# Kernel tuning notes

Hardware: AMD Instinct MI355X
Metric: run time of the kernel (lower is better)

The kernel has to match this reference:

```python
import jax, jax.numpy as jnp
import numpy as np

L, D, OC, GROUPS, EPS = 256, 1280, 128, 8, 1e-5


def setup_inputs() -> dict:
    key = jax.random.key(0)
    k1, k2 = jax.random.split(key)
    feats = jax.random.normal(k1, (L, D), dtype=jnp.float32)
    # Conv2d(3d, out_ch, kernel_size=1) weight flattened to (out_ch, 3d)
    W = jax.random.normal(k2, (OC, 3 * D), dtype=jnp.float32) * (1.0 / np.sqrt(3 * D))
    b = jnp.zeros((OC,), dtype=jnp.float32)
    gamma = jnp.ones((OC,), dtype=jnp.float32)
    beta = jnp.zeros((OC,), dtype=jnp.float32)
    return {"feats": feats, "W": W, "b": b, "gamma": gamma, "beta": beta}


def reference(feats, W, b, gamma, beta):
    fi = feats[:, None, :]                     # (L, 1, d)
    fj = feats[None, :, :]                     # (1, L, d)
    add = fi + fj                              # (L, L, d)
    diff = jnp.abs(fi - fj)                    # (L, L, d)
    had = fi * fj                              # (L, L, d)
    pair = jnp.concatenate([add, diff, had], axis=-1)  # (L, L, 3d)
    # 1x1 conv == per-pixel linear: (L, L, 3d) x (out_ch, 3d)^T -> (L, L, out_ch)
    x = jnp.einsum('ijc,oc->ijo', pair, W) + b
    # GroupNorm(8, out_ch) on batch=1: normalize over (C/g, L, L) per group
    xg = jnp.transpose(x, (2, 0, 1)).reshape(GROUPS, OC // GROUPS, L, L)
    mean = jnp.mean(xg, axis=(1, 2, 3), keepdims=True)
    var = jnp.var(xg, axis=(1, 2, 3), keepdims=True)
    xn = ((xg - mean) * jax.lax.rsqrt(var + EPS)).reshape(OC, L, L)
    xn = xn * gamma[:, None, None] + beta[:, None, None]
    out = jax.nn.gelu(xn, approximate=False)   # torch nn.GELU default = exact erf
    return out[None]                           # (1, out_ch, L, L)
```

## Files before the change

### kernel.cpp

```cpp
#include <hip/hip_runtime.h>
#include <math.h>

typedef unsigned int uint;
typedef unsigned short ushort;

typedef __attribute__((ext_vector_type(8))) _Float16 f16x8;
typedef __attribute__((ext_vector_type(2))) _Float16 f16x2;
typedef __attribute__((ext_vector_type(16))) float floatx16;

#define NFEAT 327680
#define NW    491520

union U4H8 { uint4 u; f16x8 h; uint w[4]; };

__device__ inline ushort f2h(float f) {
  _Float16 h = (_Float16)f;
  union { _Float16 h; ushort s; } c; c.h = h; return c.s;
}
__device__ inline f16x2 asf16x2(uint u) {
  union { uint u; f16x2 h; } c; c.u = u; return c.h;
}
__device__ inline uint asuint(f16x2 h) {
  union { f16x2 h; uint u; } c; c.h = h; return c.u;
}

__device__ inline void async16(const ushort* g, ushort* l) {
  __builtin_amdgcn_global_load_lds((const __attribute__((address_space(1))) uint*)g,
                                   (__attribute__((address_space(3))) uint*)l, 16, 0, 0);
}

__global__ void prep_kernel(const float* __restrict__ feats,
                            const float* __restrict__ W,
                            ushort* __restrict__ fH,
                            ushort* __restrict__ wH,
                            float* __restrict__ stats,
                            float* __restrict__ Aoi) {
  int idx = blockIdx.x * 256 + threadIdx.x;
  if (blockIdx.x == 0 && threadIdx.x < 16) stats[threadIdx.x] = 0.0f;
  if (idx < 32768) Aoi[idx] = 0.0f;
  if (idx < NFEAT) fH[idx] = f2h(feats[idx]);
  else             wH[idx - NFEAT] = f2h(W[idx - NFEAT]);
}

__global__ __launch_bounds__(256, 2) void gemma_kernel(
    const ushort* __restrict__ fH, const ushort* __restrict__ wH,
    float* __restrict__ Aoi) {
  __shared__ float red[4][1024];
  const int tid = threadIdx.x, lane = tid & 63, w = tid >> 6;
  const int i0 = (blockIdx.x >> 4) << 5;
  const int kq = (blockIdx.x >> 2) & 3;
  const int ot = blockIdx.x & 3;
  const int rr = lane & 31, half = lane >> 5;
  floatx16 a4;
  #pragma unroll
  for (int r = 0; r < 16; ++r) a4[r] = 0.0f;
  const int kbase = kq * 320 + w * 80 + half * 8;
  #pragma unroll
  for (int ks = 0; ks < 5; ++ks) {
    const int k = kbase + ks * 16;
    U4H8 bf; bf.u = *(const uint4*)(fH + (i0 + rr) * 1280 + k);
    U4H8 af; af.u = *(const uint4*)(wH + (ot * 32 + rr) * 3840 + k);
    a4 = __builtin_amdgcn_mfma_f32_32x32x16_f16(af.h, bf.h, a4, 0, 0, 0);
  }
  #pragma unroll
  for (int r = 0; r < 16; ++r) {
    const int orow = (r & 3) + 8 * (r >> 2) + 4 * half;
    red[w][orow * 32 + rr] = a4[r];
  }
  __syncthreads();
  for (int e = tid; e < 1024; e += 256) {
    float s = red[0][e] + red[1][e] + red[2][e] + red[3][e];
    atomicAdd(&Aoi[(ot * 32 + (e >> 5)) * 256 + i0 + (e & 31)], s);
  }
}

__device__ inline void build_pair(const uint4 vj, const uint4 vi, U4H8& d, U4H8& h) {
  const uint ju[4] = {vj.x, vj.y, vj.z, vj.w};
  const uint iu[4] = {vi.x, vi.y, vi.z, vi.w};
  #pragma unroll
  for (int t = 0; t < 4; ++t) {
    f16x2 a = asf16x2(iu[t]);
    f16x2 b = asf16x2(ju[t]);
    f16x2 dd = a - b;
    f16x2 hh = a * b;
    d.w[t] = asuint(dd) & 0x7fff7fffu;
    h.w[t] = asuint(hh);
  }
}

__global__ __launch_bounds__(256, 2) void gemm_kernel(
    const ushort* __restrict__ fH, const ushort* __restrict__ wH,
    const float* __restrict__ bias, const float* __restrict__ Aoi,
    float* __restrict__ xout, float* __restrict__ stats) {
  __shared__ __align__(16) ushort Wl[2 * 128 * 64];

  const int tid = threadIdx.x;
  const int blk = blockIdx.x;
  const int i0 = (blk >> 2) << 1;
  const int j0 = (blk & 3) << 6;
  const int lane = tid & 63;
  const int w = tid >> 6;
  const int wo = (w >> 1) << 6;
  const int wm = (w & 1) << 5;
  const int rr = lane & 31;
  const int half = lane >> 5;
  const int rr7 = lane & 7;

  const ushort* gsrc[4];
  #pragma unroll
  for (int p = 0; p < 4; ++p) {
    const int seg = w * 4 + p;
    const int row = seg * 8 + (lane >> 3);
    const int g = (lane & 7) ^ (lane >> 3);
    gsrc[p] = wH + row * 3840 + 1280 + (g >> 2) * 1280 + (g & 3) * 8;
  }

  const ushort* fi0p = fH + i0 * 1280 + half * 8;
  const ushort* fi1p = fi0p + 1280;
  const ushort* fjp = fH + (j0 + wm + rr) * 1280 + half * 8;

  floatx16 acc[2][2];
  #pragma unroll
  for (int a = 0; a < 2; ++a)
    #pragma unroll
    for (int ot = 0; ot < 2; ++ot)
      #pragma unroll
      for (int r = 0; r < 16; ++r) acc[a][ot][r] = 0.0f;

  #pragma unroll
  for (int p = 0; p < 4; ++p)
    async16(gsrc[p], &Wl[(w * 4 + p) * 512]);
  uint4 vi0[2], vi1[2], vj[2];
  #pragma unroll
  for (int st = 0; st < 2; ++st) {
    vj[st]  = *(const uint4*)(fjp  + st * 16);
    vi0[st] = *(const uint4*)(fi0p + st * 16);
    vi1[st] = *(const uint4*)(fi1p + st * 16);
  }
  __syncthreads();

  for (int cc = 0; cc < 40; ++cc) {
    const ushort* Wc = &Wl[(cc & 1) * 8192];
    uint4 vi0n[2], vi1n[2], vjn[2];
    if (cc < 39) {
      const int cn = (cc + 1) << 5;
      #pragma unroll
      for (int p = 0; p < 4; ++p)
        async16(gsrc[p] + cn, &Wl[((cc & 1) ^ 1) * 8192 + (w * 4 + p) * 512]);
      __builtin_amdgcn_sched_barrier(0);
      #pragma unroll
      for (int st = 0; st < 2; ++st) {
        vjn[st]  = *(const uint4*)(fjp  + cn + st * 16);
        vi0n[st] = *(const uint4*)(fi0p + cn + st * 16);
        vi1n[st] = *(const uint4*)(fi1p + cn + st * 16);
      }
      __builtin_amdgcn_sched_barrier(0);
    }
    #pragma unroll
    for (int st = 0; st < 2; ++st) {
      U4H8 d0, h0, d1, h1;
      build_pair(vj[st], vi0[st], d0, h0);
      build_pair(vj[st], vi1[st], d1, h1);
      const int g0 = (st << 1) + half;
      #pragma unroll
      for (int ot = 0; ot < 2; ++ot) {
        const int rowb = (wo + ot * 32 + rr) << 6;
        f16x8 ad = *(const f16x8*)(Wc + rowb + ((g0 ^ rr7) << 3));
        f16x8 ah = *(const f16x8*)(Wc + rowb + (((g0 + 4) ^ rr7) << 3));
        acc[0][ot] = __builtin_amdgcn_mfma_f32_32x32x16_f16(ad, d0.h, acc[0][ot], 0, 0, 0);
        acc[1][ot] = __builtin_amdgcn_mfma_f32_32x32x16_f16(ad, d1.h, acc[1][ot], 0, 0, 0);
        acc[0][ot] = __builtin_amdgcn_mfma_f32_32x32x16_f16(ah, h0.h, acc[0][ot], 0, 0, 0);
        acc[1][ot] = __builtin_amdgcn_mfma_f32_32x32x16_f16(ah, h1.h, acc[1][ot], 0, 0, 0);
      }
    }
    if (cc < 39) {
      __builtin_amdgcn_sched_barrier(0);
      __builtin_amdgcn_s_waitcnt(0x0F74);
      __builtin_amdgcn_s_barrier();
      __builtin_amdgcn_sched_barrier(0);
      __asm__ volatile("" ::: "memory");
      #pragma unroll
      for (int st = 0; st < 2; ++st) {
        vj[st] = vjn[st]; vi0[st] = vi0n[st]; vi1[st] = vi1n[st];
      }
    }
  }

  float gs[2][2] = {{0.f, 0.f}, {0.f, 0.f}};
  float gq[2][2] = {{0.f, 0.f}, {0.f, 0.f}};
  const int jg = j0 + wm + rr;
  #pragma unroll
  for (int ii = 0; ii < 2; ++ii) {
    const int irow = i0 + ii;
    const int mglob = irow * 256 + jg;
    #pragma unroll
    for (int ot = 0; ot < 2; ++ot) {
      #pragma unroll
      for (int r = 0; r < 16; ++r) {
        const int orow = (r & 3) + 8 * (r >> 2) + 4 * half;
        const int o = wo + ot * 32 + orow;
        float x = acc[ii][ot][r] + Aoi[o * 256 + irow] + Aoi[o * 256 + jg] + bias[o];
        xout[o * 65536 + mglob] = x;
        gs[ot][r >> 3] += x;
        gq[ot][r >> 3] += x * x;
      }
    }
  }
  __syncthreads();
  float* sred = (float*)Wl;
  if (tid < 16) sred[tid] = 0.0f;
  __syncthreads();
  #pragma unroll
  for (int ot = 0; ot < 2; ++ot) {
    #pragma unroll
    for (int rg = 0; rg < 2; ++rg) {
      float s = gs[ot][rg], qv = gq[ot][rg];
      for (int off = 32; off > 0; off >>= 1) {
        s += __shfl_xor(s, off, 64);
        qv += __shfl_xor(qv, off, 64);
      }
      if (lane == 0) {
        const int g = (wo >> 4) + ot * 2 + rg;
        atomicAdd(&sred[g], s);
        atomicAdd(&sred[8 + g], qv);
      }
    }
  }
  __syncthreads();
  if (tid < 16) atomicAdd(&stats[tid], sred[tid]);
}

__global__ void norm_kernel(float* __restrict__ xout,
                            const float* __restrict__ stats,
                            const float* __restrict__ gamma,
                            const float* __restrict__ beta) {
  const int idx = blockIdx.x * 256 + threadIdx.x;
  const int e = idx << 2;
  const int o = e >> 16;
  const int g = o >> 4;
  const float invN = 1.0f / 1048576.0f;
  const float mean = stats[g] * invN;
  const float var = stats[8 + g] * invN - mean * mean;
  const float inv = rsqrtf(var + 1e-5f);
  const float ga = gamma[o], be = beta[o];
  float4 v = *(float4*)(xout + e);
  float* pv = &v.x;
  #pragma unroll
  for (int t = 0; t < 4; ++t) {
    float xn = (pv[t] - mean) * inv * ga + be;
    pv[t] = 0.5f * xn * (1.0f + erff(xn * 0.70710678118654752f));
  }
  *(float4*)(xout + e) = v;
}

extern "C" void kernel_launch(void* const* d_in, const int* in_sizes, int n_in,
                              void* d_out, int out_size, void* d_ws, size_t ws_size,
                              hipStream_t stream) {
  const float* feats = (const float*)d_in[0];
  const float* W     = (const float*)d_in[1];
  const float* bias  = (const float*)d_in[2];
  const float* gamma = (const float*)d_in[3];
  const float* beta  = (const float*)d_in[4];
  float* out = (float*)d_out;

  ushort* fH = (ushort*)d_ws;
  ushort* wH = fH + NFEAT;
  float* stats = (float*)(wH + NW);
  float* Aoi = stats + 16;

  prep_kernel<<<3200, 256, 0, stream>>>(feats, W, fH, wH, stats, Aoi);
  gemma_kernel<<<128, 256, 0, stream>>>(fH, wH, Aoi);
  gemm_kernel<<<512, 256, 0, stream>>>(fH, wH, bias, Aoi, out, stats);
  norm_kernel<<<8192, 256, 0, stream>>>(out, stats, gamma, beta);
}
```

Measured before the change: 146.8 us.

## Halve gemm block tile to 32 columns and raise occupancy to four blocks per CU

Each gemm block now covers 2 rows by 32 columns of j instead of 64, and each of the four waves owns 32 output channels with a single accumulator pair instead of 64 channels split across two warps in the m dimension. The grid doubles to 1024 blocks and launch bounds ask for 4 blocks per CU, cutting accumulator registers so that more waves can be resident and the 256 CUs are better filled. The cost is that each block loads the same full 128x64 weight tile into LDS for half as much output, which doubles total weight traffic and LDS fill per unit of work.

```diff
diff --git a/kernel.cpp b/kernel.cpp
--- a/kernel.cpp
+++ b/kernel.cpp
@@ -88,7 +88,7 @@
   }
 }
 
-__global__ __launch_bounds__(256, 2) void gemm_kernel(
+__global__ __launch_bounds__(256, 4) void gemm_kernel(
     const ushort* __restrict__ fH, const ushort* __restrict__ wH,
     const float* __restrict__ bias, const float* __restrict__ Aoi,
     float* __restrict__ xout, float* __restrict__ stats) {
@@ -96,12 +96,11 @@
 
   const int tid = threadIdx.x;
   const int blk = blockIdx.x;
-  const int i0 = (blk >> 2) << 1;
-  const int j0 = (blk & 3) << 6;
+  const int i0 = (blk >> 3) << 1;
+  const int j0 = (blk & 7) << 5;
   const int lane = tid & 63;
   const int w = tid >> 6;
-  const int wo = (w >> 1) << 6;
-  const int wm = (w & 1) << 5;
+  const int wo = w << 5;
   const int rr = lane & 31;
   const int half = lane >> 5;
   const int rr7 = lane & 7;
@@ -117,15 +116,13 @@
 
   const ushort* fi0p = fH + i0 * 1280 + half * 8;
   const ushort* fi1p = fi0p + 1280;
-  const ushort* fjp = fH + (j0 + wm + rr) * 1280 + half * 8;
-
-  floatx16 acc[2][2];
+  const ushort* fjp = fH + (j0 + rr) * 1280 + half * 8;
+
+  floatx16 acc[2];
   #pragma unroll
   for (int a = 0; a < 2; ++a)
     #pragma unroll
-    for (int ot = 0; ot < 2; ++ot)
-      #pragma unroll
-      for (int r = 0; r < 16; ++r) acc[a][ot][r] = 0.0f;
+    for (int r = 0; r < 16; ++r) acc[a][r] = 0.0f;
 
   #pragma unroll
   for (int p = 0; p < 4; ++p)
@@ -162,16 +159,13 @@
       build_pair(vj[st], vi0[st], d0, h0);
       build_pair(vj[st], vi1[st], d1, h1);
       const int g0 = (st << 1) + half;
-      #pragma unroll
-      for (int ot = 0; ot < 2; ++ot) {
-        const int rowb = (wo + ot * 32 + rr) << 6;
-        f16x8 ad = *(const f16x8*)(Wc + rowb + ((g0 ^ rr7) << 3));
-        f16x8 ah = *(const f16x8*)(Wc + rowb + (((g0 + 4) ^ rr7) << 3));
-        acc[0][ot] = __builtin_amdgcn_mfma_f32_32x32x16_f16(ad, d0.h, acc[0][ot], 0, 0, 0);
-        acc[1][ot] = __builtin_amdgcn_mfma_f32_32x32x16_f16(ad, d1.h, acc[1][ot], 0, 0, 0);
-        acc[0][ot] = __builtin_amdgcn_mfma_f32_32x32x16_f16(ah, h0.h, acc[0][ot], 0, 0, 0);
-        acc[1][ot] = __builtin_amdgcn_mfma_f32_32x32x16_f16(ah, h1.h, acc[1][ot], 0, 0, 0);
-      }
+      const int rowb = (wo + rr) << 6;
+      f16x8 ad = *(const f16x8*)(Wc + rowb + ((g0 ^ rr7) << 3));
+      f16x8 ah = *(const f16x8*)(Wc + rowb + (((g0 + 4) ^ rr7) << 3));
+      acc[0] = __builtin_amdgcn_mfma_f32_32x32x16_f16(ad, d0.h, acc[0], 0, 0, 0);
+      acc[1] = __builtin_amdgcn_mfma_f32_32x32x16_f16(ad, d1.h, acc[1], 0, 0, 0);
+      acc[0] = __builtin_amdgcn_mfma_f32_32x32x16_f16(ah, h0.h, acc[0], 0, 0, 0);
+      acc[1] = __builtin_amdgcn_mfma_f32_32x32x16_f16(ah, h1.h, acc[1], 0, 0, 0);
     }
     if (cc < 39) {
       __builtin_amdgcn_sched_barrier(0);
@@ -186,24 +180,21 @@
     }
   }
 
-  float gs[2][2] = {{0.f, 0.f}, {0.f, 0.f}};
-  float gq[2][2] = {{0.f, 0.f}, {0.f, 0.f}};
-  const int jg = j0 + wm + rr;
+  float gs[2] = {0.f, 0.f};
+  float gq[2] = {0.f, 0.f};
+  const int jg = j0 + rr;
   #pragma unroll
   for (int ii = 0; ii < 2; ++ii) {
     const int irow = i0 + ii;
     const int mglob = irow * 256 + jg;
     #pragma unroll
-    for (int ot = 0; ot < 2; ++ot) {
-      #pragma unroll
-      for (int r = 0; r < 16; ++r) {
-        const int orow = (r & 3) + 8 * (r >> 2) + 4 * half;
-        const int o = wo + ot * 32 + orow;
-        float x = acc[ii][ot][r] + Aoi[o * 256 + irow] + Aoi[o * 256 + jg] + bias[o];
-        xout[o * 65536 + mglob] = x;
-        gs[ot][r >> 3] += x;
-        gq[ot][r >> 3] += x * x;
-      }
+    for (int r = 0; r < 16; ++r) {
+      const int orow = (r & 3) + 8 * (r >> 2) + 4 * half;
+      const int o = wo + orow;
+      float x = acc[ii][r] + Aoi[o * 256 + irow] + Aoi[o * 256 + jg] + bias[o];
+      xout[o * 65536 + mglob] = x;
+      gs[r >> 3] += x;
+      gq[r >> 3] += x * x;
     }
   }
   __syncthreads();
@@ -211,19 +202,16 @@
   if (tid < 16) sred[tid] = 0.0f;
   __syncthreads();
   #pragma unroll
-  for (int ot = 0; ot < 2; ++ot) {
-    #pragma unroll
-    for (int rg = 0; rg < 2; ++rg) {
-      float s = gs[ot][rg], qv = gq[ot][rg];
-      for (int off = 32; off > 0; off >>= 1) {
-        s += __shfl_xor(s, off, 64);
-        qv += __shfl_xor(qv, off, 64);
-      }
-      if (lane == 0) {
-        const int g = (wo >> 4) + ot * 2 + rg;
-        atomicAdd(&sred[g], s);
-        atomicAdd(&sred[8 + g], qv);
-      }
+  for (int rg = 0; rg < 2; ++rg) {
+    float s = gs[rg], qv = gq[rg];
+    for (int off = 32; off > 0; off >>= 1) {
+      s += __shfl_xor(s, off, 64);
+      qv += __shfl_xor(qv, off, 64);
+    }
+    if (lane == 0) {
+      const int g = (w << 1) + rg;
+      atomicAdd(&sred[g], s);
+      atomicAdd(&sred[8 + g], qv);
     }
   }
   __syncthreads();
@@ -270,6 +258,6 @@
 
   prep_kernel<<<3200, 256, 0, stream>>>(feats, W, fH, wH, stats, Aoi);
   gemma_kernel<<<128, 256, 0, stream>>>(fH, wH, Aoi);
-  gemm_kernel<<<512, 256, 0, stream>>>(fH, wH, bias, Aoi, out, stats);
+  gemm_kernel<<<1024, 256, 0, stream>>>(fH, wH, bias, Aoi, out, stats);
   norm_kernel<<<8192, 256, 0, stream>>>(out, stats, gamma, beta);
 }
```

After: 178.2 us. 1.21x slower.

## Pre-pack W into MFMA fragment layout and load directly to registers

Applied to the files above, without the earlier changes.

The prep kernel now splits W into a plain copy of the additive slice and a packed copy of the diff/hadamard slices, stored in the exact per-lane MFMA A-fragment order. The main GEMM drops the LDS double-buffer with async global-to-LDS copies and barriers. Each wave instead loads its weight fragments from global memory straight into registers, using a two-stage software pipeline of register buffers. This removes LDS traffic and block-wide syncs per chunk, but every wave re-reads weights from global/L2 and register pressure goes up.

```diff
diff --git a/kernel.cpp b/kernel.cpp
--- a/kernel.cpp
+++ b/kernel.cpp
@@ -9,7 +9,8 @@
 typedef __attribute__((ext_vector_type(16))) float floatx16;
 
 #define NFEAT 327680
-#define NW    491520
+#define NWA   163840
+#define NWP   327680
 
 union U4H8 { uint4 u; f16x8 h; uint w[4]; };
 
@@ -24,26 +25,41 @@
   union { f16x2 h; uint u; } c; c.h = h; return c.u;
 }
 
-__device__ inline void async16(const ushort* g, ushort* l) {
-  __builtin_amdgcn_global_load_lds((const __attribute__((address_space(1))) uint*)g,
-                                   (__attribute__((address_space(3))) uint*)l, 16, 0, 0);
-}
-
 __global__ void prep_kernel(const float* __restrict__ feats,
                             const float* __restrict__ W,
                             ushort* __restrict__ fH,
-                            ushort* __restrict__ wH,
+                            ushort* __restrict__ wA,
+                            ushort* __restrict__ wP,
                             float* __restrict__ stats,
                             float* __restrict__ Aoi) {
   int idx = blockIdx.x * 256 + threadIdx.x;
   if (blockIdx.x == 0 && threadIdx.x < 16) stats[threadIdx.x] = 0.0f;
   if (idx < 32768) Aoi[idx] = 0.0f;
-  if (idx < NFEAT) fH[idx] = f2h(feats[idx]);
-  else             wH[idx - NFEAT] = f2h(W[idx - NFEAT]);
+  if (idx < NFEAT) {
+    fH[idx] = f2h(feats[idx]);
+  } else {
+    const int e = idx - NFEAT;
+    const int o = e / 3840;
+    const int c = e - o * 3840;
+    const ushort v = f2h(W[e]);
+    if (c < 1280) {
+      wA[o * 1280 + c] = v;
+    } else {
+      const int cp = c - 1280;
+      const int t = cp / 1280;
+      const int kk = cp - t * 1280;
+      const int ks = kk >> 4;
+      const int khalf = (kk >> 3) & 1;
+      const int ko = kk & 7;
+      const int lane = khalf * 32 + (o & 31);
+      const int tile = (ks * 2 + t) * 4 + (o >> 5);
+      wP[tile * 512 + lane * 8 + ko] = v;
+    }
+  }
 }
 
 __global__ __launch_bounds__(256, 2) void gemma_kernel(
-    const ushort* __restrict__ fH, const ushort* __restrict__ wH,
+    const ushort* __restrict__ fH, const ushort* __restrict__ wA,
     float* __restrict__ Aoi) {
   __shared__ float red[4][1024];
   const int tid = threadIdx.x, lane = tid & 63, w = tid >> 6;
@@ -59,7 +75,7 @@
   for (int ks = 0; ks < 5; ++ks) {
     const int k = kbase + ks * 16;
     U4H8 bf; bf.u = *(const uint4*)(fH + (i0 + rr) * 1280 + k);
-    U4H8 af; af.u = *(const uint4*)(wH + (ot * 32 + rr) * 3840 + k);
+    U4H8 af; af.u = *(const uint4*)(wA + (ot * 32 + rr) * 1280 + k);
     a4 = __builtin_amdgcn_mfma_f32_32x32x16_f16(af.h, bf.h, a4, 0, 0, 0);
   }
   #pragma unroll
@@ -89,10 +105,10 @@
 }
 
 __global__ __launch_bounds__(256, 2) void gemm_kernel(
-    const ushort* __restrict__ fH, const ushort* __restrict__ wH,
+    const ushort* __restrict__ fH, const ushort* __restrict__ wP,
     const float* __restrict__ bias, const float* __restrict__ Aoi,
     float* __restrict__ xout, float* __restrict__ stats) {
-  __shared__ __align__(16) ushort Wl[2 * 128 * 64];
+  __shared__ float sred[16];
 
   const int tid = threadIdx.x;
   const int blk = blockIdx.x;
@@ -104,20 +120,11 @@
   const int wm = (w & 1) << 5;
   const int rr = lane & 31;
   const int half = lane >> 5;
-  const int rr7 = lane & 7;
-
-  const ushort* gsrc[4];
-  #pragma unroll
-  for (int p = 0; p < 4; ++p) {
-    const int seg = w * 4 + p;
-    const int row = seg * 8 + (lane >> 3);
-    const int g = (lane & 7) ^ (lane >> 3);
-    gsrc[p] = wH + row * 3840 + 1280 + (g >> 2) * 1280 + (g & 3) * 8;
-  }
-
+
+  const ushort* wpl = wP + ((wo >> 5) << 9) + lane * 8;
   const ushort* fi0p = fH + i0 * 1280 + half * 8;
   const ushort* fi1p = fi0p + 1280;
-  const ushort* fjp = fH + (j0 + wm + rr) * 1280 + half * 8;
+  const ushort* fjp  = fH + (j0 + wm + rr) * 1280 + half * 8;
 
   floatx16 acc[2][2];
   #pragma unroll
@@ -127,64 +134,53 @@
       #pragma unroll
       for (int r = 0; r < 16; ++r) acc[a][ot][r] = 0.0f;
 
-  #pragma unroll
-  for (int p = 0; p < 4; ++p)
-    async16(gsrc[p], &Wl[(w * 4 + p) * 512]);
-  uint4 vi0[2], vi1[2], vj[2];
-  #pragma unroll
-  for (int st = 0; st < 2; ++st) {
-    vj[st]  = *(const uint4*)(fjp  + st * 16);
-    vi0[st] = *(const uint4*)(fi0p + st * 16);
-    vi1[st] = *(const uint4*)(fi1p + st * 16);
-  }
-  __syncthreads();
-
-  for (int cc = 0; cc < 40; ++cc) {
-    const ushort* Wc = &Wl[(cc & 1) * 8192];
-    uint4 vi0n[2], vi1n[2], vjn[2];
-    if (cc < 39) {
-      const int cn = (cc + 1) << 5;
-      #pragma unroll
-      for (int p = 0; p < 4; ++p)
-        async16(gsrc[p] + cn, &Wl[((cc & 1) ^ 1) * 8192 + (w * 4 + p) * 512]);
-      __builtin_amdgcn_sched_barrier(0);
-      #pragma unroll
-      for (int st = 0; st < 2; ++st) {
-        vjn[st]  = *(const uint4*)(fjp  + cn + st * 16);
-        vi0n[st] = *(const uint4*)(fi0p + cn + st * 16);
-        vi1n[st] = *(const uint4*)(fi1p + cn + st * 16);
-      }
-      __builtin_amdgcn_sched_barrier(0);
-    }
-    #pragma unroll
-    for (int st = 0; st < 2; ++st) {
-      U4H8 d0, h0, d1, h1;
-      build_pair(vj[st], vi0[st], d0, h0);
-      build_pair(vj[st], vi1[st], d1, h1);
-      const int g0 = (st << 1) + half;
-      #pragma unroll
-      for (int ot = 0; ot < 2; ++ot) {
-        const int rowb = (wo + ot * 32 + rr) << 6;
-        f16x8 ad = *(const f16x8*)(Wc + rowb + ((g0 ^ rr7) << 3));
-        f16x8 ah = *(const f16x8*)(Wc + rowb + (((g0 + 4) ^ rr7) << 3));
-        acc[0][ot] = __builtin_amdgcn_mfma_f32_32x32x16_f16(ad, d0.h, acc[0][ot], 0, 0, 0);
-        acc[1][ot] = __builtin_amdgcn_mfma_f32_32x32x16_f16(ad, d1.h, acc[1][ot], 0, 0, 0);
-        acc[0][ot] = __builtin_amdgcn_mfma_f32_32x32x16_f16(ah, h0.h, acc[0][ot], 0, 0, 0);
-        acc[1][ot] = __builtin_amdgcn_mfma_f32_32x32x16_f16(ah, h1.h, acc[1][ot], 0, 0, 0);
-      }
-    }
-    if (cc < 39) {
-      __builtin_amdgcn_sched_barrier(0);
-      __builtin_amdgcn_s_waitcnt(0x0F74);
-      __builtin_amdgcn_s_barrier();
-      __builtin_amdgcn_sched_barrier(0);
-      __asm__ volatile("" ::: "memory");
-      #pragma unroll
-      for (int st = 0; st < 2; ++st) {
-        vj[st] = vjn[st]; vi0[st] = vi0n[st]; vi1[st] = vi1n[st];
-      }
-    }
-  }
+  U4H8 wfA[8], wfB[8];
+  uint4 vjA[2], viA0[2], viA1[2], vjB[2], viB0[2], viB1[2];
+
+#define CHUNK_LOAD(WF, VJ, VI0, VI1, CC) do {                                 \
+    const int _b = (CC) * 16;                                                 \
+    _Pragma("unroll")                                                         \
+    for (int _q = 0; _q < 8; ++_q) {                                          \
+      const int _st = _q >> 2, _t = (_q >> 1) & 1, _oi = _q & 1;              \
+      (WF)[_q].u = *(const uint4*)(wpl + ((_b + _st * 8 + _t * 4 + _oi) << 9)); \
+    }                                                                         \
+    const int _cb = (CC) << 5;                                                \
+    _Pragma("unroll")                                                         \
+    for (int _s = 0; _s < 2; ++_s) {                                          \
+      (VJ)[_s]  = *(const uint4*)(fjp  + _cb + _s * 16);                      \
+      (VI0)[_s] = *(const uint4*)(fi0p + _cb + _s * 16);                      \
+      (VI1)[_s] = *(const uint4*)(fi1p + _cb + _s * 16);                      \
+    }                                                                         \
+  } while (0)
+
+#define CHUNK_COMPUTE(WF, VJ, VI0, VI1) do {                                  \
+    _Pragma("unroll")                                                         \
+    for (int _s = 0; _s < 2; ++_s) {                                          \
+      U4H8 d0, h0, d1, h1;                                                    \
+      build_pair((VJ)[_s], (VI0)[_s], d0, h0);                                \
+      build_pair((VJ)[_s], (VI1)[_s], d1, h1);                                \
+      acc[0][0] = __builtin_amdgcn_mfma_f32_32x32x16_f16((WF)[_s*4+0].h, d0.h, acc[0][0], 0, 0, 0); \
+      acc[1][0] = __builtin_amdgcn_mfma_f32_32x32x16_f16((WF)[_s*4+0].h, d1.h, acc[1][0], 0, 0, 0); \
+      acc[0][1] = __builtin_amdgcn_mfma_f32_32x32x16_f16((WF)[_s*4+1].h, d0.h, acc[0][1], 0, 0, 0); \
+      acc[1][1] = __builtin_amdgcn_mfma_f32_32x32x16_f16((WF)[_s*4+1].h, d1.h, acc[1][1], 0, 0, 0); \
+      acc[0][0] = __builtin_amdgcn_mfma_f32_32x32x16_f16((WF)[_s*4+2].h, h0.h, acc[0][0], 0, 0, 0); \
+      acc[1][0] = __builtin_amdgcn_mfma_f32_32x32x16_f16((WF)[_s*4+2].h, h1.h, acc[1][0], 0, 0, 0); \
+      acc[0][1] = __builtin_amdgcn_mfma_f32_32x32x16_f16((WF)[_s*4+3].h, h0.h, acc[0][1], 0, 0, 0); \
+      acc[1][1] = __builtin_amdgcn_mfma_f32_32x32x16_f16((WF)[_s*4+3].h, h1.h, acc[1][1], 0, 0, 0); \
+    }                                                                         \
+  } while (0)
+
+  CHUNK_LOAD(wfA, vjA, viA0, viA1, 0);
+  #pragma unroll 1
+  for (int cc = 0; cc < 40; cc += 2) {
+    CHUNK_LOAD(wfB, vjB, viB0, viB1, cc + 1);
+    CHUNK_COMPUTE(wfA, vjA, viA0, viA1);
+    if (cc + 2 < 40)
+      CHUNK_LOAD(wfA, vjA, viA0, viA1, cc + 2);
+    CHUNK_COMPUTE(wfB, vjB, viB0, viB1);
+  }
+#undef CHUNK_LOAD
+#undef CHUNK_COMPUTE
 
   float gs[2][2] = {{0.f, 0.f}, {0.f, 0.f}};
   float gq[2][2] = {{0.f, 0.f}, {0.f, 0.f}};
@@ -206,8 +202,6 @@
       }
     }
   }
-  __syncthreads();
-  float* sred = (float*)Wl;
   if (tid < 16) sred[tid] = 0.0f;
   __syncthreads();
   #pragma unroll
@@ -264,12 +258,13 @@
   float* out = (float*)d_out;
 
   ushort* fH = (ushort*)d_ws;
-  ushort* wH = fH + NFEAT;
-  float* stats = (float*)(wH + NW);
+  ushort* wA = fH + NFEAT;
+  ushort* wP = wA + NWA;
+  float* stats = (float*)(wP + NWP);
   float* Aoi = stats + 16;
 
-  prep_kernel<<<3200, 256, 0, stream>>>(feats, W, fH, wH, stats, Aoi);
-  gemma_kernel<<<128, 256, 0, stream>>>(fH, wH, Aoi);
-  gemm_kernel<<<512, 256, 0, stream>>>(fH, wH, bias, Aoi, out, stats);
+  prep_kernel<<<3200, 256, 0, stream>>>(feats, W, fH, wA, wP, stats, Aoi);
+  gemma_kernel<<<128, 256, 0, stream>>>(fH, wA, Aoi);
+  gemm_kernel<<<512, 256, 0, stream>>>(fH, wP, bias, Aoi, out, stats);
   norm_kernel<<<8192, 256, 0, stream>>>(out, stats, gamma, beta);
 }
```

Result: no change. 144.4 us (-1.6%).
